# Kernel optimization log

Measured on AMD Instinct MI355X. Metric: run time of the kernel, lower is better.

The kernel has to match this reference:

```python
import jax, jax.numpy as jnp
import numpy as np
import math

B, S, IN, D, H, L, DFF = 8, 512, 32, 512, 8, 6, 2048
DK = D // H
LN_EPS = 1e-5
KL_EPS = 1e-8


def _pos_encoding(seq_len, d_model):
    pe = np.zeros((seq_len, d_model), dtype=np.float32)
    pos = np.arange(seq_len, dtype=np.float32)[:, None]
    div = np.exp(np.arange(0, d_model, 2, dtype=np.float32) * (-math.log(10000.0) / d_model))
    pe[:, 0::2] = np.sin(pos * div)
    pe[:, 1::2] = np.cos(pos * div)
    return jnp.asarray(pe)


def setup_inputs() -> dict:
    key = jax.random.key(0)
    ks = iter(jax.random.split(key, 32))
    g = lambda shape: jax.random.normal(next(ks), shape, dtype=jnp.float32) * 0.02
    return {
        'x': jax.random.normal(next(ks), (B, S, IN), dtype=jnp.float32),
        'W_in': g((IN, D)), 'b_in': jnp.zeros((D,), jnp.float32),
        'pe': _pos_encoding(S, D),
        'Wq': g((L, D, D)), 'Wk': g((L, D, D)), 'Wv': g((L, D, D)),
        'Wo': g((L, D, D)), 'bo': jnp.zeros((L, D), jnp.float32),
        'W1': g((L, D, DFF)), 'b1': jnp.zeros((L, DFF), jnp.float32),
        'W2': g((L, DFF, D)), 'b2': jnp.zeros((L, D), jnp.float32),
        'ln1_g': jnp.ones((L, D), jnp.float32), 'ln1_b': jnp.zeros((L, D), jnp.float32),
        'ln2_g': jnp.ones((L, D), jnp.float32), 'ln2_b': jnp.zeros((L, D), jnp.float32),
        'W_out': g((D, IN)), 'b_out': jnp.zeros((IN,), jnp.float32),
        'Ws1': g((D, D // 2)), 'bs1': jnp.zeros((D // 2,), jnp.float32),
        'Ws2': g((D // 2, 1)), 'bs2': jnp.zeros((1,), jnp.float32),
    }


def _layernorm(v, gamma, beta):
    mu = v.mean(-1, keepdims=True)
    var = ((v - mu) ** 2).mean(-1, keepdims=True)
    return (v - mu) * jax.lax.rsqrt(var + LN_EPS) * gamma + beta


def reference(x, W_in, b_in, pe, Wq, Wk, Wv, Wo, bo, W1, b1, W2, b2,
              ln1_g, ln1_b, ln2_g, ln2_b, W_out, b_out, Ws1, bs1, Ws2, bs2):
    b, s, _ = x.shape
    h = x @ W_in + b_in + pe[None, :s, :]
    total_assoc = jnp.zeros((b, s), x.dtype)
    scale = 1.0 / math.sqrt(DK)
    prior = 1.0 / s + KL_EPS
    for l in range(L):
        # QKV: [b, h, s, dk]
        Q = (h @ Wq[l]).reshape(b, s, H, DK).transpose(0, 2, 1, 3)
        K = (h @ Wk[l]).reshape(b, s, H, DK).transpose(0, 2, 1, 3)
        V = (h @ Wv[l]).reshape(b, s, H, DK).transpose(0, 2, 1, 3)
        scores = jnp.einsum('bhsk,bhtk->bhst', Q, K) * scale
        attn = jax.nn.softmax(scores, axis=-1)  # [b,h,s,s]
        ctx = jnp.einsum('bhst,bhtk->bhsk', attn, V)
        ctx = ctx.transpose(0, 2, 1, 3).reshape(b, s, D)
        attn_out = ctx @ Wo[l] + bo[l]
        # association discrepancy: KL(avg_attn || uniform prior) per query
        avg_attn = attn.mean(axis=1) + KL_EPS  # [b,s,s]
        total_assoc = total_assoc + (avg_attn * jnp.log(avg_attn / prior)).sum(-1)
        h = _layernorm(h + attn_out, ln1_g[l], ln1_b[l])
        ff = jax.nn.relu(h @ W1[l] + b1[l]) @ W2[l] + b2[l]
        h = _layernorm(h + ff, ln2_g[l], ln2_b[l])
    reconstruction = h @ W_out + b_out
    anomaly_scores = jax.nn.sigmoid(jax.nn.relu(h @ Ws1 + bs1) @ Ws2 + bs2)[..., 0]
    avg_association = total_assoc / L
    return reconstruction, anomaly_scores, avg_association
```

## Files before the change

### kernel.cpp

```cpp
#include <hip/hip_runtime.h>
#include <math.h>

typedef __attribute__((ext_vector_type(8))) short bf16x8;
typedef __attribute__((ext_vector_type(4))) float f32x4;

__device__ __forceinline__ short f2bf(float v) {
  union { float f; unsigned u; } x; x.f = v;
  unsigned r = x.u + 0x7fffu + ((x.u >> 16) & 1u);
  return (short)(r >> 16);
}

__device__ __forceinline__ float bf2f(unsigned short u) {
  union { unsigned u; float f; } x; x.u = ((unsigned)u) << 16;
  return x.f;
}

__device__ __forceinline__ void gld_lds16(const void* g, void* l) {
  __builtin_amdgcn_global_load_lds((const __attribute__((address_space(1))) void*)g,
                                   (__attribute__((address_space(3))) void*)l, 16, 0, 0);
}

__global__ __launch_bounds__(256) void transpose_bf(const float* __restrict__ src,
                                                    short* __restrict__ dst,
                                                    int R, int C, size_t sStride, size_t dStride) {
  __shared__ float t[32][33];
  src += blockIdx.z * sStride;
  dst += blockIdx.z * dStride;
  int tx = threadIdx.x & 31, ty = threadIdx.x >> 5;
  int c0 = blockIdx.x * 32, r0 = blockIdx.y * 32;
#pragma unroll
  for (int i = 0; i < 4; i++)
    t[ty + i * 8][tx] = src[(size_t)(r0 + ty + i * 8) * C + c0 + tx];
  __syncthreads();
#pragma unroll
  for (int i = 0; i < 4; i++)
    dst[(size_t)(c0 + ty + i * 8) * R + r0 + tx] = f2bf(t[tx][ty + i * 8]);
}

__global__ __launch_bounds__(256) void transpose_qkv(const float* __restrict__ Wq,
                                                     const float* __restrict__ Wk,
                                                     const float* __restrict__ Wv,
                                                     short* __restrict__ qkvt) {
  __shared__ float t[32][33];
  const int z = blockIdx.z;
  const int which = z / 6, l = z % 6;
  const float* src = (which == 0 ? Wq : which == 1 ? Wk : Wv) + (size_t)l * 262144;
  short* dst = qkvt + (size_t)l * 786432 + (size_t)which * 262144;
  int tx = threadIdx.x & 31, ty = threadIdx.x >> 5;
  int c0 = blockIdx.x * 32, r0 = blockIdx.y * 32;
#pragma unroll
  for (int i = 0; i < 4; i++)
    t[ty + i * 8][tx] = src[(size_t)(r0 + ty + i * 8) * 512 + c0 + tx];
  __syncthreads();
#pragma unroll
  for (int i = 0; i < 4; i++)
    dst[(size_t)(c0 + ty + i * 8) * 512 + r0 + tx] = f2bf(t[tx][ty + i * 8]);
}

__global__ void embed_kernel(const float* __restrict__ x, const float* __restrict__ W_in,
                             const float* __restrict__ b_in, const float* __restrict__ pe,
                             float* __restrict__ h, short* __restrict__ hbf) {
  int col = (blockIdx.x & 1) * 256 + threadIdx.x;
  int row = blockIdx.x >> 1;
  int s = row & 511;
  float a = b_in[col] + pe[s * 512 + col];
  const float* xr = x + (size_t)row * 32;
#pragma unroll
  for (int k = 0; k < 32; k++) a += xr[k] * W_in[k * 512 + col];
  h[(size_t)row * 512 + col] = a;
  hbf[(size_t)row * 512 + col] = f2bf(a);
}

template <int EPI, int BM, int BN, int BK>
__global__ __launch_bounds__(256) void gemm_bt(const short* __restrict__ A,
                                               const short* __restrict__ Bt,
                                               float* __restrict__ Cf, short* __restrict__ Cb,
                                               const float* __restrict__ bias,
                                               int M, int N, int K) {
  __shared__ short As[BM * BK];
  __shared__ short Bs[BN * BK];
  const int tid = threadIdx.x;
  const int wid = tid >> 6;
  const int lane = tid & 63;
  const int m0 = blockIdx.y * BM;
  const int n0 = blockIdx.x * BN;
  constexpr int WR = BM / 2, WC = BN / 2, FI = WR / 16, FJ = WC / 16, KK = BK / 32;
  const int wr = (wid >> 1) * WR;
  const int wc = (wid & 1) * WC;

  f32x4 acc[FI][FJ];
#pragma unroll
  for (int i = 0; i < FI; i++)
#pragma unroll
    for (int j = 0; j < FJ; j++)
#pragma unroll
      for (int q = 0; q < 4; q++) acc[i][j][q] = 0.0f;

  const short* aBase = A + (size_t)m0 * K;
  const short* bBase = Bt + (size_t)n0 * K;
  constexpr int RPC = 512 / BK;
  constexpr int CA = BM / RPC;
  constexpr int CT = (BM + BN) / RPC;
  const int rowL = lane / (64 / RPC);
  const int colE = (lane % (64 / RPC)) * 8;
  const int kg = (lane >> 4) * 8;
  const int r16 = lane & 15;

  for (int kt = 0; kt < K; kt += BK) {
    __syncthreads();
#pragma unroll
    for (int c = 0; c < CT / 4; ++c) {
      int s = c * 4 + wid;
      if (s < CA)
        gld_lds16(aBase + (size_t)(s * RPC + rowL) * K + kt + colE, As + s * 512);
      else
        gld_lds16(bBase + (size_t)((s - CA) * RPC + rowL) * K + kt + colE, Bs + (s - CA) * 512);
    }
    __syncthreads();
    bf16x8 af[FI][KK], bfr[FJ][KK];
#pragma unroll
    for (int i = 0; i < FI; i++)
#pragma unroll
      for (int kk = 0; kk < KK; kk++)
        af[i][kk] = *(const bf16x8*)&As[(wr + i * 16 + r16) * BK + kk * 32 + kg];
#pragma unroll
    for (int j = 0; j < FJ; j++)
#pragma unroll
      for (int kk = 0; kk < KK; kk++)
        bfr[j][kk] = *(const bf16x8*)&Bs[(wc + j * 16 + r16) * BK + kk * 32 + kg];
#pragma unroll
    for (int kk = 0; kk < KK; kk++)
#pragma unroll
      for (int i = 0; i < FI; i++)
#pragma unroll
        for (int j = 0; j < FJ; j++)
          acc[i][j] = __builtin_amdgcn_mfma_f32_16x16x32_bf16(af[i][kk], bfr[j][kk], acc[i][j], 0, 0, 0);
  }

  const int col16 = lane & 15;
  const int rowg = (lane >> 4) * 4;
#pragma unroll
  for (int i = 0; i < FI; i++) {
    int row = m0 + wr + i * 16 + rowg;
#pragma unroll
    for (int j = 0; j < FJ; j++) {
      int col = n0 + wc + j * 16 + col16;
      float bv = (EPI == 1 || EPI == 2 || EPI == 4) ? bias[col] : 0.0f;
#pragma unroll
      for (int q = 0; q < 4; q++) {
        float v = acc[i][j][q] + bv;
        if (EPI == 2) {
          v = fmaxf(v, 0.0f);
          Cb[(size_t)(row + q) * N + col] = f2bf(v);
        } else if (EPI == 3 || EPI == 4) {
          Cb[(size_t)(row + q) * N + col] = f2bf(v);
        } else {
          Cf[(size_t)(row + q) * N + col] = v;
        }
      }
    }
  }
}

__global__ __launch_bounds__(256) void sm_kernel(const short* __restrict__ qkvh,
                                                 short* __restrict__ P) {
  const int bh = blockIdx.y, b = bh >> 3, h = bh & 7;
  const int q0 = blockIdx.x * 64;
  const int wid = threadIdx.x >> 6, lane = threadIdx.x & 63;
  const int r16 = lane & 15, g = lane >> 4;

  const short* qp = qkvh + (size_t)(b * 512 + q0 + wid * 16 + r16) * 1536 + h * 64 + g * 8;
  const bf16x8 qa0 = *(const bf16x8*)qp;
  const bf16x8 qa1 = *(const bf16x8*)(qp + 32);

  const short* kbase = qkvh + (size_t)(b * 512) * 1536 + 512 + h * 64 + g * 8;

  f32x4 acc[32];
#pragma unroll
  for (int tt = 0; tt < 32; ++tt) {
    const short* kp = kbase + (size_t)(tt * 16 + r16) * 1536;
    bf16x8 kb0 = *(const bf16x8*)kp;
    bf16x8 kb1 = *(const bf16x8*)(kp + 32);
    f32x4 c = {0.f, 0.f, 0.f, 0.f};
    c = __builtin_amdgcn_mfma_f32_16x16x32_bf16(qa0, kb0, c, 0, 0, 0);
    c = __builtin_amdgcn_mfma_f32_16x16x32_bf16(qa1, kb1, c, 0, 0, 0);
    acc[tt] = c;
  }

  float mx[4] = {-1e30f, -1e30f, -1e30f, -1e30f};
#pragma unroll
  for (int tt = 0; tt < 32; ++tt)
#pragma unroll
    for (int r = 0; r < 4; ++r) mx[r] = fmaxf(mx[r], acc[tt][r]);
#pragma unroll
  for (int r = 0; r < 4; ++r)
#pragma unroll
    for (int m = 8; m; m >>= 1) mx[r] = fmaxf(mx[r], __shfl_xor(mx[r], m, 16));

  float sum[4] = {0.f, 0.f, 0.f, 0.f};
#pragma unroll
  for (int tt = 0; tt < 32; ++tt)
#pragma unroll
    for (int r = 0; r < 4; ++r) {
      float e = __expf((acc[tt][r] - mx[r]) * 0.125f);
      sum[r] += e;
      acc[tt][r] = e;
    }
#pragma unroll
  for (int r = 0; r < 4; ++r)
#pragma unroll
    for (int m = 8; m; m >>= 1) sum[r] += __shfl_xor(sum[r], m, 16);
  float inv[4];
#pragma unroll
  for (int r = 0; r < 4; ++r) inv[r] = 1.0f / sum[r];

  short* prow = P + ((size_t)bh * 512 + q0 + wid * 16 + g * 4) * 512 + r16;
#pragma unroll
  for (int r = 0; r < 4; ++r)
#pragma unroll
    for (int tt = 0; tt < 32; ++tt)
      prow[(size_t)r * 512 + tt * 16] = f2bf(acc[tt][r] * inv[r]);
}

__global__ __launch_bounds__(256) void vt_kernel(const short* __restrict__ qkvh,
                                                 short* __restrict__ Vt) {
  __shared__ short t[32][34];
  const int bh = blockIdx.z, b = bh >> 3, h = bh & 7;
  const int t0 = blockIdx.x * 32, d0 = blockIdx.y * 32;
  const int tx = threadIdx.x & 31, ty = threadIdx.x >> 5;
#pragma unroll
  for (int i = 0; i < 4; i++)
    t[ty + i * 8][tx] = qkvh[(size_t)(b * 512 + t0 + ty + i * 8) * 1536 + 1024 + h * 64 + d0 + tx];
  __syncthreads();
#pragma unroll
  for (int i = 0; i < 4; i++)
    Vt[((size_t)bh * 64 + d0 + ty + i * 8) * 512 + t0 + tx] = t[tx][ty + i * 8];
}

__global__ __launch_bounds__(256) void pv_gemm(const short* __restrict__ P,
                                               const short* __restrict__ Vt,
                                               short* __restrict__ ctxb) {
  __shared__ short As[128 * 32];
  __shared__ short Bs[64 * 32];
  const int bh = blockIdx.y, b = bh >> 3, h = bh & 7;
  const int m0 = blockIdx.x * 128;
  const int tid = threadIdx.x, wid = tid >> 6, lane = tid & 63;
  const short* aBase = P + ((size_t)bh * 512 + m0) * 512;
  const short* bBase = Vt + (size_t)bh * 64 * 512;
  const int rowA0 = lane >> 2, colE = (lane & 3) * 8, kg = (lane >> 4) * 8, r16 = lane & 15;

  f32x4 acc[2][4];
#pragma unroll
  for (int i = 0; i < 2; i++)
#pragma unroll
    for (int j = 0; j < 4; j++)
#pragma unroll
      for (int q = 0; q < 4; q++) acc[i][j][q] = 0.0f;

  for (int kt = 0; kt < 512; kt += 32) {
    __syncthreads();
    gld_lds16(aBase + (size_t)(wid * 16 + rowA0) * 512 + kt + colE, As + wid * 512);
    gld_lds16(aBase + (size_t)((wid + 4) * 16 + rowA0) * 512 + kt + colE, As + (wid + 4) * 512);
    gld_lds16(bBase + (size_t)(wid * 16 + rowA0) * 512 + kt + colE, Bs + wid * 512);
    __syncthreads();
    bf16x8 af[2], bfr[4];
#pragma unroll
    for (int i = 0; i < 2; i++)
      af[i] = *(const bf16x8*)&As[(wid * 32 + i * 16 + r16) * 32 + kg];
#pragma unroll
    for (int j = 0; j < 4; j++)
      bfr[j] = *(const bf16x8*)&Bs[(j * 16 + r16) * 32 + kg];
#pragma unroll
    for (int i = 0; i < 2; i++)
#pragma unroll
      for (int j = 0; j < 4; j++)
        acc[i][j] = __builtin_amdgcn_mfma_f32_16x16x32_bf16(af[i], bfr[j], acc[i][j], 0, 0, 0);
  }

  const int rowg = (lane >> 4) * 4;
#pragma unroll
  for (int i = 0; i < 2; i++) {
    int row = m0 + wid * 32 + i * 16 + rowg;
#pragma unroll
    for (int j = 0; j < 4; j++) {
      int col = h * 64 + j * 16 + r16;
#pragma unroll
      for (int q = 0; q < 4; q++)
        ctxb[(size_t)(b * 512 + row + q) * 512 + col] = f2bf(acc[i][j][q]);
    }
  }
}

template <int FIRST>
__global__ __launch_bounds__(256) void kl_kernel(const short* __restrict__ P,
                                                 float* __restrict__ assoc) {
  const int wid = threadIdx.x >> 6, lane = threadIdx.x & 63;
  const int row = blockIdx.x * 4 + wid;
  const int b = row >> 9, q = row & 511;
  const float prior = 1.0f / 512.0f + 1e-8f;
  float hs[8] = {0.f, 0.f, 0.f, 0.f, 0.f, 0.f, 0.f, 0.f};
#pragma unroll
  for (int h = 0; h < 8; ++h) {
    bf16x8 v = *(const bf16x8*)&P[(((size_t)(b * 8 + h)) * 512 + q) * 512 + lane * 8];
#pragma unroll
    for (int k = 0; k < 8; ++k) hs[k] += bf2f((unsigned short)v[k]);
  }
  float s = 0.f;
#pragma unroll
  for (int k = 0; k < 8; ++k) {
    float a = hs[k] * 0.125f + 1e-8f;
    s += a * __logf(a / prior);
  }
#pragma unroll
  for (int m = 32; m; m >>= 1) s += __shfl_xor(s, m, 64);
  if (lane == 0) assoc[row] = FIRST ? s : (assoc[row] + s);
}

__global__ __launch_bounds__(256) void ln_kernel(const float* __restrict__ hin,
                                                 const short* __restrict__ res,
                                                 const float* __restrict__ g,
                                                 const float* __restrict__ bta,
                                                 float* __restrict__ hout, short* __restrict__ hbf) {
  const int wid = threadIdx.x >> 6, lane = threadIdx.x & 63;
  const size_t row = (size_t)blockIdx.x * 4 + wid;
  const float* hp = hin + row * 512;
  const short* rp = res + row * 512;
  float v[8], s = 0.f, s2 = 0.f;
#pragma unroll
  for (int i = 0; i < 8; i++) {
    int c = lane + i * 64;
    v[i] = hp[c] + bf2f((unsigned short)rp[c]);
    s += v[i];
    s2 += v[i] * v[i];
  }
#pragma unroll
  for (int m = 32; m; m >>= 1) {
    s += __shfl_xor(s, m, 64);
    s2 += __shfl_xor(s2, m, 64);
  }
  float mu = s * (1.0f / 512.0f);
  float var = s2 * (1.0f / 512.0f) - mu * mu;
  float rs = rsqrtf(var + 1e-5f);
#pragma unroll
  for (int i = 0; i < 8; i++) {
    int c = lane + i * 64;
    float y = (v[i] - mu) * rs * g[c] + bta[c];
    hout[row * 512 + c] = y;
    hbf[row * 512 + c] = f2bf(y);
  }
}

__global__ __launch_bounds__(256) void recon_mfma(const short* __restrict__ hbf,
                                                  const short* __restrict__ WoutT,
                                                  const float* __restrict__ bout,
                                                  float* __restrict__ out) {
  const int wid = threadIdx.x >> 6, lane = threadIdx.x & 63;
  const int r16 = lane & 15, kg = (lane >> 4) * 8;
  const int wbase = blockIdx.x * 128 + wid * 32;

  f32x4 acc[2][2];
#pragma unroll
  for (int i = 0; i < 2; i++)
#pragma unroll
    for (int j = 0; j < 2; j++)
#pragma unroll
      for (int q = 0; q < 4; q++) acc[i][j][q] = 0.0f;

  for (int kt = 0; kt < 512; kt += 32) {
    bf16x8 af[2], bfr[2];
#pragma unroll
    for (int i = 0; i < 2; i++)
      af[i] = *(const bf16x8*)&hbf[(size_t)(wbase + i * 16 + r16) * 512 + kt + kg];
#pragma unroll
    for (int j = 0; j < 2; j++)
      bfr[j] = *(const bf16x8*)&WoutT[(size_t)(j * 16 + r16) * 512 + kt + kg];
#pragma unroll
    for (int i = 0; i < 2; i++)
#pragma unroll
      for (int j = 0; j < 2; j++)
        acc[i][j] = __builtin_amdgcn_mfma_f32_16x16x32_bf16(af[i], bfr[j], acc[i][j], 0, 0, 0);
  }

  const int rowg = (lane >> 4) * 4;
#pragma unroll
  for (int i = 0; i < 2; i++)
#pragma unroll
    for (int j = 0; j < 2; j++) {
      int col = j * 16 + r16;
#pragma unroll
      for (int q = 0; q < 4; q++)
        out[(size_t)(wbase + i * 16 + rowg + q) * 32 + col] = acc[i][j][q] + bout[col];
    }
}

__global__ __launch_bounds__(256) void score2_kernel(const short* __restrict__ s1,
                                                     const float* __restrict__ Ws2,
                                                     const float* __restrict__ bs2,
                                                     const float* __restrict__ assoc,
                                                     float* __restrict__ outScore,
                                                     float* __restrict__ outAssoc) {
  const int wid = threadIdx.x >> 6, lane = threadIdx.x & 63;
  const int row = blockIdx.x * 4 + wid;
  const short* rp = &s1[(size_t)row * 256 + lane * 4];
  float d = 0.f;
#pragma unroll
  for (int e = 0; e < 4; e++) d += bf2f((unsigned short)rp[e]) * Ws2[lane * 4 + e];
#pragma unroll
  for (int m = 32; m; m >>= 1) d += __shfl_xor(d, m, 64);
  if (lane == 0) {
    outScore[row] = 1.f / (1.f + __expf(-(d + bs2[0])));
    outAssoc[row] = assoc[row] * (1.0f / 6.0f);
  }
}

extern "C" void kernel_launch(void* const* d_in, const int* in_sizes, int n_in,
                              void* d_out, int out_size, void* d_ws, size_t ws_size,
                              hipStream_t stream) {
  const float* x    = (const float*)d_in[0];
  const float* W_in = (const float*)d_in[1];
  const float* b_in = (const float*)d_in[2];
  const float* pe   = (const float*)d_in[3];
  const float* Wq   = (const float*)d_in[4];
  const float* Wk   = (const float*)d_in[5];
  const float* Wv   = (const float*)d_in[6];
  const float* Wo   = (const float*)d_in[7];
  const float* bo   = (const float*)d_in[8];
  const float* W1   = (const float*)d_in[9];
  const float* b1   = (const float*)d_in[10];
  const float* W2   = (const float*)d_in[11];
  const float* b2   = (const float*)d_in[12];
  const float* ln1g = (const float*)d_in[13];
  const float* ln1b = (const float*)d_in[14];
  const float* ln2g = (const float*)d_in[15];
  const float* ln2b = (const float*)d_in[16];
  const float* Wout = (const float*)d_in[17];
  const float* bout = (const float*)d_in[18];
  const float* Ws1  = (const float*)d_in[19];
  const float* bs1  = (const float*)d_in[20];
  const float* Ws2  = (const float*)d_in[21];
  const float* bs2  = (const float*)d_in[22];

  char* p = (char*)d_ws;
  auto alloc = [&](size_t bytes) {
    void* r = (void*)p;
    p += (bytes + 255) & ~(size_t)255;
    return r;
  };
  float* h     = (float*)alloc((size_t)4096 * 512 * 4);
  short* h_bf  = (short*)alloc((size_t)4096 * 512 * 2);
  short* qkvh  = (short*)alloc((size_t)4096 * 1536 * 2);
  short* aout  = (short*)alloc((size_t)4096 * 512 * 2);
  short* ctxb  = (short*)alloc((size_t)4096 * 512 * 2);
  short* ff1b  = (short*)alloc((size_t)4096 * 2048 * 2);
  short* ff2   = (short*)alloc((size_t)4096 * 512 * 2);
  float* assoc = (float*)alloc((size_t)4096 * 4);
  short* Pbuf  = (short*)alloc((size_t)64 * 512 * 512 * 2);
  short* Vt    = (short*)alloc((size_t)64 * 64 * 512 * 2);
  short* sc1   = (short*)alloc((size_t)4096 * 256 * 2);
  short* qkvt  = (short*)alloc((size_t)6 * 1536 * 512 * 2);
  short* wot   = (short*)alloc((size_t)6 * 512 * 512 * 2);
  short* w1t   = (short*)alloc((size_t)6 * 2048 * 512 * 2);
  short* w2t   = (short*)alloc((size_t)6 * 512 * 2048 * 2);
  short* ws1t  = (short*)alloc((size_t)256 * 512 * 2);
  short* woutT = (short*)alloc((size_t)32 * 512 * 2);

  transpose_qkv<<<dim3(16, 16, 18), 256, 0, stream>>>(Wq, Wk, Wv, qkvt);
  transpose_bf<<<dim3(16, 16, 6), 256, 0, stream>>>(Wo, wot, 512, 512, 262144, 262144);
  transpose_bf<<<dim3(64, 16, 6), 256, 0, stream>>>(W1, w1t, 512, 2048, 1048576, 1048576);
  transpose_bf<<<dim3(16, 64, 6), 256, 0, stream>>>(W2, w2t, 2048, 512, 1048576, 1048576);
  transpose_bf<<<dim3(8, 16, 1), 256, 0, stream>>>(Ws1, ws1t, 512, 256, 0, 0);
  transpose_bf<<<dim3(1, 16, 1), 256, 0, stream>>>(Wout, woutT, 512, 32, 0, 0);

  embed_kernel<<<8192, 256, 0, stream>>>(x, W_in, b_in, pe, h, h_bf);

  for (int l = 0; l < 6; ++l) {
    gemm_bt<3, 128, 128, 32><<<dim3(12, 32), 256, 0, stream>>>(
        h_bf, qkvt + (size_t)l * 786432, nullptr, qkvh, nullptr, 4096, 1536, 512);
    vt_kernel<<<dim3(16, 2, 64), 256, 0, stream>>>(qkvh, Vt);
    sm_kernel<<<dim3(8, 64), 256, 0, stream>>>(qkvh, Pbuf);
    pv_gemm<<<dim3(4, 64), 256, 0, stream>>>(Pbuf, Vt, ctxb);
    if (l == 0)
      kl_kernel<1><<<1024, 256, 0, stream>>>(Pbuf, assoc);
    else
      kl_kernel<0><<<1024, 256, 0, stream>>>(Pbuf, assoc);
    gemm_bt<4, 64, 64, 32><<<dim3(8, 64), 256, 0, stream>>>(
        ctxb, wot + (size_t)l * 262144, nullptr, aout, bo + l * 512, 4096, 512, 512);
    ln_kernel<<<1024, 256, 0, stream>>>(h, aout, ln1g + l * 512, ln1b + l * 512, h, h_bf);
    gemm_bt<2, 128, 128, 32><<<dim3(16, 32), 256, 0, stream>>>(
        h_bf, w1t + (size_t)l * 1048576, nullptr, ff1b, b1 + l * 2048, 4096, 2048, 512);
    gemm_bt<4, 64, 64, 32><<<dim3(8, 64), 256, 0, stream>>>(
        ff1b, w2t + (size_t)l * 1048576, nullptr, ff2, b2 + l * 512, 4096, 512, 2048);
    ln_kernel<<<1024, 256, 0, stream>>>(h, ff2, ln2g + l * 512, ln2b + l * 512, h, h_bf);
  }

  float* out = (float*)d_out;
  recon_mfma<<<32, 256, 0, stream>>>(h_bf, woutT, bout, out);
  gemm_bt<2, 128, 128, 32><<<dim3(2, 32), 256, 0, stream>>>(h_bf, ws1t, nullptr, sc1, bs1,
                                                            4096, 256, 512);
  score2_kernel<<<1024, 256, 0, stream>>>(sc1, Ws2, bs2, assoc, out + 131072,
                                          out + 131072 + 4096);
}
```

Before: 887.3 us.

## Fuse softmax with PV matmul via LDS and vectorize layernorm accesses

Softmax probabilities are staged in a swizzled 64KB LDS tile, written to global with coalesced 16-byte stores for the KL kernel, and then used directly as the A operand of the PV MFMA inside the same kernel. This removes the separate pv_gemm launch and its re-read of P from global memory. The layernorm kernel is also switched to per-lane contiguous vectorized loads and stores. The 64KB LDS allocation limits occupancy, and the fused PV loop reads Vt straight from global with no LDS staging.

New measurement: 909.9 us. +2.5%, slower.

```diff
diff --git a/kernel.cpp b/kernel.cpp
--- a/kernel.cpp
+++ b/kernel.cpp
@@ -3,6 +3,7 @@
 
 typedef __attribute__((ext_vector_type(8))) short bf16x8;
 typedef __attribute__((ext_vector_type(4))) float f32x4;
+typedef __attribute__((ext_vector_type(4))) float float4v;
 
 __device__ __forceinline__ short f2bf(float v) {
   union { float f; unsigned u; } x; x.f = v;
@@ -162,8 +163,11 @@
   }
 }
 
-__global__ __launch_bounds__(256) void sm_kernel(const short* __restrict__ qkvh,
-                                                 short* __restrict__ P) {
+__global__ __launch_bounds__(256) void smpv_kernel(const short* __restrict__ qkvh,
+                                                   const short* __restrict__ Vt,
+                                                   short* __restrict__ P,
+                                                   short* __restrict__ ctxb) {
+  __shared__ short Pl[64 * 512];
   const int bh = blockIdx.y, b = bh >> 3, h = bh & 7;
   const int q0 = blockIdx.x * 64;
   const int wid = threadIdx.x >> 6, lane = threadIdx.x & 63;
@@ -172,7 +176,6 @@
   const short* qp = qkvh + (size_t)(b * 512 + q0 + wid * 16 + r16) * 1536 + h * 64 + g * 8;
   const bf16x8 qa0 = *(const bf16x8*)qp;
   const bf16x8 qa1 = *(const bf16x8*)(qp + 32);
-
   const short* kbase = qkvh + (size_t)(b * 512) * 1536 + 512 + h * 64 + g * 8;
 
   f32x4 acc[32];
@@ -214,12 +217,56 @@
 #pragma unroll
   for (int r = 0; r < 4; ++r) inv[r] = 1.0f / sum[r];
 
-  short* prow = P + ((size_t)bh * 512 + q0 + wid * 16 + g * 4) * 512 + r16;
-#pragma unroll
-  for (int r = 0; r < 4; ++r)
-#pragma unroll
-    for (int tt = 0; tt < 32; ++tt)
-      prow[(size_t)r * 512 + tt * 16] = f2bf(acc[tt][r] * inv[r]);
+  char* plc = (char*)Pl;
+#pragma unroll
+  for (int r = 0; r < 4; ++r) {
+    const int qr = wid * 16 + g * 4 + r;
+    const int swz = (qr & 7) << 4;
+#pragma unroll
+    for (int tt = 0; tt < 32; ++tt) {
+      int tB = (tt * 16 + r16) * 2;
+      *(short*)(plc + qr * 1024 + (tB ^ swz)) = f2bf(acc[tt][r] * inv[r]);
+    }
+  }
+  __syncthreads();
+
+  short* pg = P + ((size_t)bh * 512 + q0) * 512;
+#pragma unroll
+  for (int k = 0; k < 16; ++k) {
+    int c = k * 256 + threadIdx.x;
+    int qr = c >> 6;
+    int tB = (c & 63) * 16;
+    bf16x8 v = *(const bf16x8*)(plc + qr * 1024 + (tB ^ ((qr & 7) << 4)));
+    *(bf16x8*)&pg[(size_t)qr * 512 + tB / 2] = v;
+  }
+
+  f32x4 pacc[4];
+#pragma unroll
+  for (int j = 0; j < 4; ++j)
+#pragma unroll
+    for (int q = 0; q < 4; ++q) pacc[j][q] = 0.0f;
+
+  const short* vb = Vt + (size_t)bh * 64 * 512;
+  const int qr = wid * 16 + r16;
+  const int swz = (qr & 7) << 4;
+  for (int kt = 0; kt < 512; kt += 32) {
+    int tB = (kt + g * 8) * 2;
+    bf16x8 af = *(const bf16x8*)(plc + qr * 1024 + (tB ^ swz));
+#pragma unroll
+    for (int j = 0; j < 4; ++j) {
+      bf16x8 bfr = *(const bf16x8*)&vb[(size_t)(j * 16 + r16) * 512 + kt + g * 8];
+      pacc[j] = __builtin_amdgcn_mfma_f32_16x16x32_bf16(af, bfr, pacc[j], 0, 0, 0);
+    }
+  }
+
+  const int rowg = g * 4;
+#pragma unroll
+  for (int j = 0; j < 4; ++j) {
+    int col = h * 64 + j * 16 + r16;
+#pragma unroll
+    for (int q = 0; q < 4; ++q)
+      ctxb[(size_t)(b * 512 + q0 + wid * 16 + rowg + q) * 512 + col] = f2bf(pacc[j][q]);
+  }
 }
 
 __global__ __launch_bounds__(256) void vt_kernel(const short* __restrict__ qkvh,
@@ -235,60 +282,6 @@
 #pragma unroll
   for (int i = 0; i < 4; i++)
     Vt[((size_t)bh * 64 + d0 + ty + i * 8) * 512 + t0 + tx] = t[tx][ty + i * 8];
-}
-
-__global__ __launch_bounds__(256) void pv_gemm(const short* __restrict__ P,
-                                               const short* __restrict__ Vt,
-                                               short* __restrict__ ctxb) {
-  __shared__ short As[128 * 32];
-  __shared__ short Bs[64 * 32];
-  const int bh = blockIdx.y, b = bh >> 3, h = bh & 7;
-  const int m0 = blockIdx.x * 128;
-  const int tid = threadIdx.x, wid = tid >> 6, lane = tid & 63;
-  const short* aBase = P + ((size_t)bh * 512 + m0) * 512;
-  const short* bBase = Vt + (size_t)bh * 64 * 512;
-  const int rowA0 = lane >> 2, colE = (lane & 3) * 8, kg = (lane >> 4) * 8, r16 = lane & 15;
-
-  f32x4 acc[2][4];
-#pragma unroll
-  for (int i = 0; i < 2; i++)
-#pragma unroll
-    for (int j = 0; j < 4; j++)
-#pragma unroll
-      for (int q = 0; q < 4; q++) acc[i][j][q] = 0.0f;
-
-  for (int kt = 0; kt < 512; kt += 32) {
-    __syncthreads();
-    gld_lds16(aBase + (size_t)(wid * 16 + rowA0) * 512 + kt + colE, As + wid * 512);
-    gld_lds16(aBase + (size_t)((wid + 4) * 16 + rowA0) * 512 + kt + colE, As + (wid + 4) * 512);
-    gld_lds16(bBase + (size_t)(wid * 16 + rowA0) * 512 + kt + colE, Bs + wid * 512);
-    __syncthreads();
-    bf16x8 af[2], bfr[4];
-#pragma unroll
-    for (int i = 0; i < 2; i++)
-      af[i] = *(const bf16x8*)&As[(wid * 32 + i * 16 + r16) * 32 + kg];
-#pragma unroll
-    for (int j = 0; j < 4; j++)
-      bfr[j] = *(const bf16x8*)&Bs[(j * 16 + r16) * 32 + kg];
-#pragma unroll
-    for (int i = 0; i < 2; i++)
-#pragma unroll
-      for (int j = 0; j < 4; j++)
-        acc[i][j] = __builtin_amdgcn_mfma_f32_16x16x32_bf16(af[i], bfr[j], acc[i][j], 0, 0, 0);
-  }
-
-  const int rowg = (lane >> 4) * 4;
-#pragma unroll
-  for (int i = 0; i < 2; i++) {
-    int row = m0 + wid * 32 + i * 16 + rowg;
-#pragma unroll
-    for (int j = 0; j < 4; j++) {
-      int col = h * 64 + j * 16 + r16;
-#pragma unroll
-      for (int q = 0; q < 4; q++)
-        ctxb[(size_t)(b * 512 + row + q) * 512 + col] = f2bf(acc[i][j][q]);
-    }
-  }
 }
 
 template <int FIRST>
@@ -323,13 +316,15 @@
                                                  float* __restrict__ hout, short* __restrict__ hbf) {
   const int wid = threadIdx.x >> 6, lane = threadIdx.x & 63;
   const size_t row = (size_t)blockIdx.x * 4 + wid;
-  const float* hp = hin + row * 512;
-  const short* rp = res + row * 512;
+  const float* hp = hin + row * 512 + lane * 8;
+  float4v a0 = *(const float4v*)hp;
+  float4v a1 = *(const float4v*)(hp + 4);
+  bf16x8 rv = *(const bf16x8*)(res + row * 512 + lane * 8);
   float v[8], s = 0.f, s2 = 0.f;
 #pragma unroll
   for (int i = 0; i < 8; i++) {
-    int c = lane + i * 64;
-    v[i] = hp[c] + bf2f((unsigned short)rp[c]);
+    float base = (i < 4) ? a0[i] : a1[i - 4];
+    v[i] = base + bf2f((unsigned short)rv[i]);
     s += v[i];
     s2 += v[i] * v[i];
   }
@@ -341,13 +336,20 @@
   float mu = s * (1.0f / 512.0f);
   float var = s2 * (1.0f / 512.0f) - mu * mu;
   float rs = rsqrtf(var + 1e-5f);
+  const float* gp = g + lane * 8;
+  const float* bp = bta + lane * 8;
+  float4v o0, o1;
+  bf16x8 ob;
 #pragma unroll
   for (int i = 0; i < 8; i++) {
-    int c = lane + i * 64;
-    float y = (v[i] - mu) * rs * g[c] + bta[c];
-    hout[row * 512 + c] = y;
-    hbf[row * 512 + c] = f2bf(y);
-  }
+    float y = (v[i] - mu) * rs * gp[i] + bp[i];
+    if (i < 4) o0[i] = y; else o1[i - 4] = y;
+    ob[i] = f2bf(y);
+  }
+  float* op = hout + row * 512 + lane * 8;
+  *(float4v*)op = o0;
+  *(float4v*)(op + 4) = o1;
+  *(bf16x8*)(hbf + row * 512 + lane * 8) = ob;
 }
 
 __global__ __launch_bounds__(256) void recon_mfma(const short* __restrict__ hbf,
@@ -477,8 +479,7 @@
     gemm_bt<3, 128, 128, 32><<<dim3(12, 32), 256, 0, stream>>>(
         h_bf, qkvt + (size_t)l * 786432, nullptr, qkvh, nullptr, 4096, 1536, 512);
     vt_kernel<<<dim3(16, 2, 64), 256, 0, stream>>>(qkvh, Vt);
-    sm_kernel<<<dim3(8, 64), 256, 0, stream>>>(qkvh, Pbuf);
-    pv_gemm<<<dim3(4, 64), 256, 0, stream>>>(Pbuf, Vt, ctxb);
+    smpv_kernel<<<dim3(8, 64), 256, 0, stream>>>(qkvh, Vt, Pbuf, ctxb);
     if (l == 0)
       kl_kernel<1><<<1024, 256, 0, stream>>>(Pbuf, assoc);
     else
```

## Write QKV head-major, fuse V transpose into softmax kernel, vectorize layernorm

Applied to the files above, without the earlier changes.

The QKV GEMM epilogue now scatters its output into a head-major [section][b*h][t][dk] layout, so Q and K rows for a head are contiguous. The V transpose is folded into the softmax kernel, which removes one launch per layer. The layernorm kernel now uses vector loads and stores of 8 contiguous elements per lane. The scattered GEMM epilogue stores may be less coalesced than before, and the softmax blocks now carry extra transpose work with syncthreads.

New measurement: 864.9 us. -2.5%, faster.

```diff
diff --git a/kernel.cpp b/kernel.cpp
--- a/kernel.cpp
+++ b/kernel.cpp
@@ -3,6 +3,7 @@
 
 typedef __attribute__((ext_vector_type(8))) short bf16x8;
 typedef __attribute__((ext_vector_type(4))) float f32x4;
+typedef __attribute__((ext_vector_type(4))) float float4v;
 
 __device__ __forceinline__ short f2bf(float v) {
   union { float f; unsigned u; } x; x.f = v;
@@ -152,6 +153,11 @@
         if (EPI == 2) {
           v = fmaxf(v, 0.0f);
           Cb[(size_t)(row + q) * N + col] = f2bf(v);
+        } else if (EPI == 5) {
+          int rr = row + q;
+          int sect = col >> 9, hh = (col >> 6) & 7, dk = col & 63;
+          int bq = rr >> 9, tt = rr & 511;
+          Cb[(((size_t)(sect * 64 + bq * 8 + hh)) * 512 + tt) * 64 + dk] = f2bf(v);
         } else if (EPI == 3 || EPI == 4) {
           Cb[(size_t)(row + q) * N + col] = f2bf(v);
         } else {
@@ -162,23 +168,44 @@
   }
 }
 
-__global__ __launch_bounds__(256) void sm_kernel(const short* __restrict__ qkvh,
-                                                 short* __restrict__ P) {
-  const int bh = blockIdx.y, b = bh >> 3, h = bh & 7;
+__global__ __launch_bounds__(256) void smvt_kernel(const short* __restrict__ qh,
+                                                   short* __restrict__ P,
+                                                   short* __restrict__ Vt) {
+  __shared__ short tb[32][34];
+  const int bh = blockIdx.y;
   const int q0 = blockIdx.x * 64;
-  const int wid = threadIdx.x >> 6, lane = threadIdx.x & 63;
+  const int tid = threadIdx.x;
+  const int wid = tid >> 6, lane = tid & 63;
   const int r16 = lane & 15, g = lane >> 4;
 
-  const short* qp = qkvh + (size_t)(b * 512 + q0 + wid * 16 + r16) * 1536 + h * 64 + g * 8;
+  {
+    const short* Vh = qh + ((size_t)(128 + bh) * 512) * 64;
+    const int tx = tid & 31, ty = tid >> 5;
+#pragma unroll
+    for (int i = 0; i < 4; ++i) {
+      const int idx = blockIdx.x * 4 + i;
+      const int t0 = (idx & 15) * 32, d0 = (idx >> 4) * 32;
+      __syncthreads();
+#pragma unroll
+      for (int r = 0; r < 4; ++r)
+        tb[ty + r * 8][tx] = Vh[(size_t)(t0 + ty + r * 8) * 64 + d0 + tx];
+      __syncthreads();
+#pragma unroll
+      for (int r = 0; r < 4; ++r)
+        Vt[((size_t)bh * 64 + d0 + ty + r * 8) * 512 + t0 + tx] = tb[tx][ty + r * 8];
+    }
+  }
+
+  const short* Qh = qh + ((size_t)bh * 512) * 64;
+  const short* Kh = qh + ((size_t)(64 + bh) * 512) * 64;
+  const short* qp = Qh + (size_t)(q0 + wid * 16 + r16) * 64 + g * 8;
   const bf16x8 qa0 = *(const bf16x8*)qp;
   const bf16x8 qa1 = *(const bf16x8*)(qp + 32);
 
-  const short* kbase = qkvh + (size_t)(b * 512) * 1536 + 512 + h * 64 + g * 8;
-
   f32x4 acc[32];
 #pragma unroll
   for (int tt = 0; tt < 32; ++tt) {
-    const short* kp = kbase + (size_t)(tt * 16 + r16) * 1536;
+    const short* kp = Kh + (size_t)(tt * 16 + r16) * 64 + g * 8;
     bf16x8 kb0 = *(const bf16x8*)kp;
     bf16x8 kb1 = *(const bf16x8*)(kp + 32);
     f32x4 c = {0.f, 0.f, 0.f, 0.f};
@@ -220,21 +247,6 @@
 #pragma unroll
     for (int tt = 0; tt < 32; ++tt)
       prow[(size_t)r * 512 + tt * 16] = f2bf(acc[tt][r] * inv[r]);
-}
-
-__global__ __launch_bounds__(256) void vt_kernel(const short* __restrict__ qkvh,
-                                                 short* __restrict__ Vt) {
-  __shared__ short t[32][34];
-  const int bh = blockIdx.z, b = bh >> 3, h = bh & 7;
-  const int t0 = blockIdx.x * 32, d0 = blockIdx.y * 32;
-  const int tx = threadIdx.x & 31, ty = threadIdx.x >> 5;
-#pragma unroll
-  for (int i = 0; i < 4; i++)
-    t[ty + i * 8][tx] = qkvh[(size_t)(b * 512 + t0 + ty + i * 8) * 1536 + 1024 + h * 64 + d0 + tx];
-  __syncthreads();
-#pragma unroll
-  for (int i = 0; i < 4; i++)
-    Vt[((size_t)bh * 64 + d0 + ty + i * 8) * 512 + t0 + tx] = t[tx][ty + i * 8];
 }
 
 __global__ __launch_bounds__(256) void pv_gemm(const short* __restrict__ P,
@@ -323,13 +335,15 @@
                                                  float* __restrict__ hout, short* __restrict__ hbf) {
   const int wid = threadIdx.x >> 6, lane = threadIdx.x & 63;
   const size_t row = (size_t)blockIdx.x * 4 + wid;
-  const float* hp = hin + row * 512;
-  const short* rp = res + row * 512;
+  const float* hp = hin + row * 512 + lane * 8;
+  float4v a0 = *(const float4v*)hp;
+  float4v a1 = *(const float4v*)(hp + 4);
+  bf16x8 rv = *(const bf16x8*)(res + row * 512 + lane * 8);
   float v[8], s = 0.f, s2 = 0.f;
 #pragma unroll
   for (int i = 0; i < 8; i++) {
-    int c = lane + i * 64;
-    v[i] = hp[c] + bf2f((unsigned short)rp[c]);
+    float base = (i < 4) ? a0[i] : a1[i - 4];
+    v[i] = base + bf2f((unsigned short)rv[i]);
     s += v[i];
     s2 += v[i] * v[i];
   }
@@ -341,13 +355,20 @@
   float mu = s * (1.0f / 512.0f);
   float var = s2 * (1.0f / 512.0f) - mu * mu;
   float rs = rsqrtf(var + 1e-5f);
+  const float* gp = g + lane * 8;
+  const float* bp = bta + lane * 8;
+  float4v o0, o1;
+  bf16x8 ob;
 #pragma unroll
   for (int i = 0; i < 8; i++) {
-    int c = lane + i * 64;
-    float y = (v[i] - mu) * rs * g[c] + bta[c];
-    hout[row * 512 + c] = y;
-    hbf[row * 512 + c] = f2bf(y);
-  }
+    float y = (v[i] - mu) * rs * gp[i] + bp[i];
+    if (i < 4) o0[i] = y; else o1[i - 4] = y;
+    ob[i] = f2bf(y);
+  }
+  float* op = hout + row * 512 + lane * 8;
+  *(float4v*)op = o0;
+  *(float4v*)(op + 4) = o1;
+  *(bf16x8*)(hbf + row * 512 + lane * 8) = ob;
 }
 
 __global__ __launch_bounds__(256) void recon_mfma(const short* __restrict__ hbf,
@@ -448,7 +469,7 @@
   };
   float* h     = (float*)alloc((size_t)4096 * 512 * 4);
   short* h_bf  = (short*)alloc((size_t)4096 * 512 * 2);
-  short* qkvh  = (short*)alloc((size_t)4096 * 1536 * 2);
+  short* qh    = (short*)alloc((size_t)4096 * 1536 * 2);
   short* aout  = (short*)alloc((size_t)4096 * 512 * 2);
   short* ctxb  = (short*)alloc((size_t)4096 * 512 * 2);
   short* ff1b  = (short*)alloc((size_t)4096 * 2048 * 2);
@@ -474,10 +495,9 @@
   embed_kernel<<<8192, 256, 0, stream>>>(x, W_in, b_in, pe, h, h_bf);
 
   for (int l = 0; l < 6; ++l) {
-    gemm_bt<3, 128, 128, 32><<<dim3(12, 32), 256, 0, stream>>>(
-        h_bf, qkvt + (size_t)l * 786432, nullptr, qkvh, nullptr, 4096, 1536, 512);
-    vt_kernel<<<dim3(16, 2, 64), 256, 0, stream>>>(qkvh, Vt);
-    sm_kernel<<<dim3(8, 64), 256, 0, stream>>>(qkvh, Pbuf);
+    gemm_bt<5, 128, 128, 32><<<dim3(12, 32), 256, 0, stream>>>(
+        h_bf, qkvt + (size_t)l * 786432, nullptr, qh, nullptr, 4096, 1536, 512);
+    smvt_kernel<<<dim3(8, 64), 256, 0, stream>>>(qh, Pbuf, Vt);
     pv_gemm<<<dim3(4, 64), 256, 0, stream>>>(Pbuf, Vt, ctxb);
     if (l == 0)
       kl_kernel<1><<<1024, 256, 0, stream>>>(Pbuf, assoc);
```
